# Kernel tuning notes

Measured on AMD Instinct MI355X. Metric: run time of the kernel, lower is better.

## Reference

```python
import jax, jax.numpy as jnp
import numpy as np

HIDDEN = 1024
HEADS = 16
HEAD = HIDDEN // HEADS
B, S = 2, 2048


def setup_inputs() -> dict:
    key = jax.random.key(0)
    ks = jax.random.split(key, 8)
    query = jax.random.normal(ks[0], (B, S, HIDDEN), dtype=jnp.float32)
    key_t = jax.random.normal(ks[1], (B, S, HIDDEN), dtype=jnp.float32)
    value = jax.random.normal(ks[2], (B, S, HIDDEN), dtype=jnp.float32)
    # causal mask, broadcastable over batch and heads; 0 -> masked (-inf)
    mask = jnp.tril(jnp.ones((S, S), dtype=jnp.int32))[None, None, :, :]
    # torch Linear weights are [out_features, in_features]
    scale = 0.02
    Wq = jax.random.normal(ks[3], (HIDDEN, HIDDEN), dtype=jnp.float32) * scale
    Wk = jax.random.normal(ks[4], (HIDDEN, HIDDEN), dtype=jnp.float32) * scale
    Wv = jax.random.normal(ks[5], (HIDDEN, HIDDEN), dtype=jnp.float32) * scale
    Wo = jax.random.normal(ks[6], (HIDDEN, HIDDEN), dtype=jnp.float32) * scale
    bo = jax.random.normal(ks[7], (HIDDEN,), dtype=jnp.float32) * scale
    return {"query": query, "key": key_t, "value": value, "mask": mask,
            "Wq": Wq, "Wk": Wk, "Wv": Wv, "Wo": Wo, "bo": bo}


def reference(query, key, value, mask, Wq, Wk, Wv, Wo, bo):
    b = query.shape[0]
    # Linear (no bias): x @ W^T, then split into heads -> [b, h, s, d]
    def heads(x, W):
        y = jnp.einsum('bse,oe->bso', x, W)
        return y.reshape(b, -1, HEADS, HEAD).transpose(0, 2, 1, 3)
    Q = heads(query, Wq)
    K = heads(key, Wk)
    V = heads(value, Wv)
    inv_scale = 1.0 / jnp.sqrt(jnp.float32(HEAD))
    scores = jnp.einsum('bhqd,bhkd->bhqk', Q, K) * inv_scale  # [b,h,s,s]
    scores = jnp.where(mask == 0, -jnp.inf, scores)
    attn = jax.nn.softmax(scores, axis=-1)
    x = jnp.einsum('bhqk,bhkd->bhqd', attn, V)
    x = x.transpose(0, 2, 1, 3).reshape(b, -1, HIDDEN)
    return jnp.einsum('bse,oe->bso', x, Wo) + bo
```

## Files before the change

### kernel.cpp

```cpp
#include <hip/hip_runtime.h>


typedef __attribute__((ext_vector_type(8))) short short8;
typedef __attribute__((ext_vector_type(4))) float f32x4;
typedef unsigned int u32;
typedef unsigned short u16;

__device__ inline f32x4 mfma16(short8 a, short8 b, f32x4 c) {
    return __builtin_amdgcn_mfma_f32_16x16x32_bf16(a, b, c, 0, 0, 0);
}
__device__ inline u16 f2bf(float f) {
    union { float f; u32 u; } v; v.f = f;
    u32 r = v.u + 0x7fff + ((v.u >> 16) & 1);
    return (u16)(r >> 16);
}
__device__ inline void gll16(void* lds, const void* g) {
    __builtin_amdgcn_global_load_lds((const __attribute__((address_space(1))) u32*)g,
                                     (__attribute__((address_space(3))) u32*)lds,
                                     16, 0, 0);
}
__device__ inline u32 pkbf(float hi, float lo) {
    return __builtin_amdgcn_perm(__float_as_uint(hi), __float_as_uint(lo),
                                 0x07060302u);
}

__global__ __launch_bounds__(256)
void cvt_all(const float* __restrict__ q, const float* __restrict__ k,
             const float* __restrict__ v, const float* __restrict__ wq,
             const float* __restrict__ wk, const float* __restrict__ wv,
             const float* __restrict__ wo,
             u16* __restrict__ q16, u16* __restrict__ k16,
             u16* __restrict__ v16, u16* __restrict__ w16) {
    const size_t QKV = 1u << 22;
    const size_t WSZ = 1u << 20;
    size_t base = ((size_t)blockIdx.x * 256 + threadIdx.x) * 8;
    const float* src; u16* dst; size_t off; float scale = 1.0f;
    if (base < QKV)            { src = q; dst = q16; off = base;
                                 scale = 0.125f * 1.44269504f; }
    else if (base < 2 * QKV)   { src = k; dst = k16; off = base - QKV;     }
    else if (base < 3 * QKV)   { src = v; dst = v16; off = base - 2 * QKV; }
    else {
        size_t wb = base - 3 * QKV;
        int wi = (int)(wb >> 20); off = wb & (WSZ - 1);
        src = wi == 0 ? wq : wi == 1 ? wk : wi == 2 ? wv : wo;
        dst = w16 + (size_t)wi * WSZ;
    }
    float4 f0 = *(const float4*)(src + off);
    float4 f1 = *(const float4*)(src + off + 4);
    short8 s = { (short)f2bf(f0.x * scale), (short)f2bf(f0.y * scale),
                 (short)f2bf(f0.z * scale), (short)f2bf(f0.w * scale),
                 (short)f2bf(f1.x * scale), (short)f2bf(f1.y * scale),
                 (short)f2bf(f1.z * scale), (short)f2bf(f1.w * scale) };
    *(short8*)(dst + off) = s;
}

__global__ __launch_bounds__(256)
void gemm_qkv(const u16* __restrict__ q16, const u16* __restrict__ k16,
              const u16* __restrict__ v16, const u16* __restrict__ w16,
              u16* __restrict__ Qg, u16* __restrict__ Kg, u16* __restrict__ Vt) {
    const int K = 1024;
    __shared__ u16 As[3][128 * 32];
    __shared__ u16 Bs[3][128 * 32];
    const int z = blockIdx.z;
    const u16* A = z == 0 ? q16 : z == 1 ? k16 : v16;
    const u16* W = w16 + (size_t)z * (1u << 20);

    const int tid = threadIdx.x, lane = tid & 63, w = tid >> 6;
    const int ln15 = lane & 15, quad = lane >> 4;
    const int fr = (ln15 >> 1) & 3;
    const int lrow = lane >> 2;
    const int lcs = (((lane & 3) ^ ((lane >> 3) & 3)) << 3);
    const int m0 = blockIdx.y * 128, n0 = blockIdx.x * 128;
    const int wm = (w >> 1) * 64, wn = (w & 1) * 64;

    f32x4 acc[4][4] = {};

    #pragma unroll
    for (int t = 0; t < 2; ++t)
        #pragma unroll
        for (int c = 0; c < 2; ++c) {
            gll16(&As[t][(w * 32 + c * 16) * 32],
                  &A[(size_t)(m0 + w * 32 + c * 16 + lrow) * K + t * 32 + lcs]);
            gll16(&Bs[t][(w * 32 + c * 16) * 32],
                  &W[(size_t)(n0 + w * 32 + c * 16 + lrow) * K + t * 32 + lcs]);
        }

    int cur = 0;
    for (int t = 0; t < 32; ++t) {
        if (t < 31) {
            __asm__ volatile("s_waitcnt vmcnt(4)" ::: "memory");
        } else {
            __asm__ volatile("s_waitcnt vmcnt(0)" ::: "memory");
        }
        __builtin_amdgcn_s_barrier();
        __builtin_amdgcn_sched_barrier(0);

        if (t < 30) {
            const int k0 = (t + 2) * 32;
            const int nb = (cur + 2 >= 3) ? cur - 1 : cur + 2;
            #pragma unroll
            for (int c = 0; c < 2; ++c) {
                gll16(&As[nb][(w * 32 + c * 16) * 32],
                      &A[(size_t)(m0 + w * 32 + c * 16 + lrow) * K + k0 + lcs]);
                gll16(&Bs[nb][(w * 32 + c * 16) * 32],
                      &W[(size_t)(n0 + w * 32 + c * 16 + lrow) * K + k0 + lcs]);
            }
        }
        __builtin_amdgcn_sched_barrier(0);

        short8 a[4], b[4];
        #pragma unroll
        for (int mt = 0; mt < 4; ++mt)
            a[mt] = *(const short8*)&As[cur][(wm + mt * 16 + ln15) * 32 +
                                            ((quad ^ fr) << 3)];
        #pragma unroll
        for (int nt = 0; nt < 4; ++nt)
            b[nt] = *(const short8*)&Bs[cur][(wn + nt * 16 + ln15) * 32 +
                                            ((quad ^ fr) << 3)];
        #pragma unroll
        for (int mt = 0; mt < 4; ++mt)
            #pragma unroll
            for (int nt = 0; nt < 4; ++nt)
                acc[mt][nt] = mfma16(a[mt], b[nt], acc[mt][nt]);

        cur = (cur == 2) ? 0 : cur + 1;
    }

    #pragma unroll
    for (int mt = 0; mt < 4; ++mt)
        #pragma unroll
        for (int nt = 0; nt < 4; ++nt)
            #pragma unroll
            for (int r = 0; r < 4; ++r) {
                int m = m0 + wm + mt * 16 + quad * 4 + r;
                int n = n0 + wn + nt * 16 + ln15;
                u16 hv = f2bf(acc[mt][nt][r]);
                if (z == 2) {
                    int b_ = m >> 11, s_ = m & 2047, h_ = n >> 6, d_ = n & 63;
                    int kl = s_ & 63;
                    int sp = (s_ & ~63) + (kl & 15) * 4 + (kl >> 4);
                    Vt[((size_t)(b_ * 16 + h_) * 64 + d_) * 2048 + sp] = hv;
                } else {
                    u16* dst = z ? Kg : Qg;
                    dst[(size_t)m * 1024 + n] = hv;
                }
            }
}

__global__ __launch_bounds__(256)
void gemm_out(const u16* __restrict__ A, const u16* __restrict__ W,
              const float* __restrict__ bias, float* __restrict__ out) {
    const int K = 1024;
    __shared__ u16 As[3][64 * 64];
    __shared__ u16 Bs[3][128 * 64];
    const int id = blockIdx.x;
    const int by = id >> 3, bx = id & 7;

    const int tid = threadIdx.x, lane = tid & 63, w = tid >> 6;
    const int ln15 = lane & 15, quad = lane >> 4, s7 = ln15 & 7;
    const int lr = lane >> 3;
    const int lcs = (((lane & 7) ^ lr) << 3);
    const int m0 = by * 64, n0 = bx * 128;
    const int wm = (w & 1) * 32, wn = (w >> 1) * 64;

    f32x4 acc[2][4] = {};

    #pragma unroll
    for (int t = 0; t < 2; ++t) {
        #pragma unroll
        for (int c = 0; c < 2; ++c)
            gll16(&As[t][(w * 16 + c * 8) * 64],
                  &A[(size_t)(m0 + w * 16 + c * 8 + lr) * K + t * 64 + lcs]);
        #pragma unroll
        for (int c = 0; c < 4; ++c)
            gll16(&Bs[t][(w * 32 + c * 8) * 64],
                  &W[(size_t)(n0 + w * 32 + c * 8 + lr) * K + t * 64 + lcs]);
    }

    int cur = 0;
    for (int i = 0; i < 16; ++i) {
        if (i < 15) {
            __asm__ volatile("s_waitcnt vmcnt(6)" ::: "memory");
        } else {
            __asm__ volatile("s_waitcnt vmcnt(0)" ::: "memory");
        }
        __builtin_amdgcn_s_barrier();
        __builtin_amdgcn_sched_barrier(0);

        if (i < 14) {
            const int k0 = (i + 2) * 64;
            const int nb = (cur + 2 >= 3) ? cur - 1 : cur + 2;
            #pragma unroll
            for (int c = 0; c < 2; ++c)
                gll16(&As[nb][(w * 16 + c * 8) * 64],
                      &A[(size_t)(m0 + w * 16 + c * 8 + lr) * K + k0 + lcs]);
            #pragma unroll
            for (int c = 0; c < 4; ++c)
                gll16(&Bs[nb][(w * 32 + c * 8) * 64],
                      &W[(size_t)(n0 + w * 32 + c * 8 + lr) * K + k0 + lcs]);
        }
        __builtin_amdgcn_sched_barrier(0);

        #pragma unroll
        for (int kh = 0; kh < 2; ++kh) {
            short8 a[2], b[4];
            #pragma unroll
            for (int mt = 0; mt < 2; ++mt)
                a[mt] = *(const short8*)&As[cur][(wm + mt * 16 + ln15) * 64 +
                                                (((kh * 4 + quad) ^ s7) << 3)];
            #pragma unroll
            for (int nt = 0; nt < 4; ++nt)
                b[nt] = *(const short8*)&Bs[cur][(wn + nt * 16 + ln15) * 64 +
                                                (((kh * 4 + quad) ^ s7) << 3)];
            #pragma unroll
            for (int mt = 0; mt < 2; ++mt)
                #pragma unroll
                for (int nt = 0; nt < 4; ++nt)
                    acc[mt][nt] = mfma16(a[mt], b[nt], acc[mt][nt]);
        }
        cur = (cur == 2) ? 0 : cur + 1;
    }

    #pragma unroll
    for (int mt = 0; mt < 2; ++mt)
        #pragma unroll
        for (int nt = 0; nt < 4; ++nt)
            #pragma unroll
            for (int r = 0; r < 4; ++r) {
                int m = m0 + wm + mt * 16 + quad * 4 + r;
                int n = n0 + wn + nt * 16 + ln15;
                out[(size_t)m * 1024 + n] = acc[mt][nt][r] + bias[n];
            }
}

__global__ __launch_bounds__(256)
void attn3(const u16* __restrict__ Qg, const u16* __restrict__ Kg,
           const u16* __restrict__ Vt, u16* __restrict__ Xb) {
    __shared__ u16 Kl[3][64 * 64];
    __shared__ u16 Vl[3][64 * 64];
    __shared__ u16 Pl[4][16 * 72];

    const int id = blockIdx.x;
    const int bh = id & 31, qt = 31 - (id >> 5);
    const int b = bh >> 4, h = bh & 15;
    const int tid = threadIdx.x, lane = tid & 63, w = tid >> 6;
    const int ln15 = lane & 15, quad = lane >> 4, s7 = ln15 & 7;
    const int lr = lane >> 3;
    const int lcs = (((lane & 7) ^ lr) << 3);
    const u16* Kbase = Kg + (size_t)b * 2048 * 1024 + h * 64;
    const u16* Vbase = Vt + (size_t)bh * 64 * 2048;
    const float M0L = 8.65617025f;
    const int q0 = qt * 64;

    const u16* qrow = Qg + (size_t)(b * 2048 + q0 + w * 16 + ln15) * 1024 + h * 64;
    short8 aq0 = *(const short8*)(qrow + quad * 8);
    short8 aq1 = *(const short8*)(qrow + 32 + quad * 8);
    __asm__ volatile("s_waitcnt vmcnt(0)" ::: "memory");

    f32x4 o[4] = {};
    float lsum[4] = {0.f, 0.f, 0.f, 0.f};

    #pragma unroll
    for (int c = 0; c < 2; ++c) {
        const int r0 = w * 16 + c * 8;
        gll16(&Kl[0][r0 * 64], Kbase + (size_t)(r0 + lr) * 1024 + lcs);
        gll16(&Vl[0][r0 * 64], Vbase + (size_t)(r0 + lr) * 2048 + lcs);
    }
    if (qt >= 1) {
        #pragma unroll
        for (int c = 0; c < 2; ++c) {
            const int r0 = w * 16 + c * 8;
            gll16(&Kl[1][r0 * 64], Kbase + (size_t)(64 + r0 + lr) * 1024 + lcs);
            gll16(&Vl[1][r0 * 64], Vbase + (size_t)(r0 + lr) * 2048 + 64 + lcs);
        }
    }

    int cur = 0;
    for (int kt = 0; kt <= qt; ++kt) {
        if (kt < qt) {
            __asm__ volatile("s_waitcnt vmcnt(4)" ::: "memory");
        } else {
            __asm__ volatile("s_waitcnt vmcnt(0)" ::: "memory");
        }
        __builtin_amdgcn_s_barrier();
        __builtin_amdgcn_sched_barrier(0);

        if (kt + 2 <= qt) {
            const int nk = (kt + 2) * 64;
            const int nb = (cur + 2 >= 3) ? cur - 1 : cur + 2;
            #pragma unroll
            for (int c = 0; c < 2; ++c) {
                const int r0 = w * 16 + c * 8;
                gll16(&Kl[nb][r0 * 64], Kbase + (size_t)(nk + r0 + lr) * 1024 + lcs);
                gll16(&Vl[nb][r0 * 64], Vbase + (size_t)(r0 + lr) * 2048 + nk + lcs);
            }
        }
        __builtin_amdgcn_sched_barrier(0);

        f32x4 sc[4];
        #pragma unroll
        for (int ct = 0; ct < 4; ++ct) {
            short8 b0 = *(const short8*)&Kl[cur][(ct * 16 + ln15) * 64 +
                                                ((quad ^ s7) << 3)];
            short8 b1 = *(const short8*)&Kl[cur][(ct * 16 + ln15) * 64 +
                                                (((4 + quad) ^ s7) << 3)];
            f32x4 c = {};
            c = mfma16(aq0, b0, c);
            c = mfma16(aq1, b1, c);
            sc[ct] = c;
        }

        const bool diag = (kt == qt);
        #pragma unroll
        for (int r = 0; r < 4; ++r) {
            float s0 = sc[0][r], s1 = sc[1][r], s2 = sc[2][r], s3 = sc[3][r];
            if (diag) {
                const int qq = w * 16 + quad * 4 + r;
                s0 = (ln15      <= qq) ? s0 : -1e30f;
                s1 = (16 + ln15 <= qq) ? s1 : -1e30f;
                s2 = (32 + ln15 <= qq) ? s2 : -1e30f;
                s3 = (48 + ln15 <= qq) ? s3 : -1e30f;
            }
            float p0 = __builtin_amdgcn_exp2f(s0 - M0L);
            float p1 = __builtin_amdgcn_exp2f(s1 - M0L);
            float p2 = __builtin_amdgcn_exp2f(s2 - M0L);
            float p3 = __builtin_amdgcn_exp2f(s3 - M0L);
            uint2 pw = make_uint2(pkbf(p1, p0), pkbf(p3, p2));
            *(uint2*)&Pl[w][(quad * 4 + r) * 72 + ln15 * 4] = pw;
            lsum[r] += (p0 + p1) + (p2 + p3);
        }

        __asm__ volatile("s_waitcnt lgkmcnt(0)" ::: "memory");
        short8 ap0 = *(const short8*)&Pl[w][ln15 * 72 + quad * 8];
        short8 ap1 = *(const short8*)&Pl[w][ln15 * 72 + 32 + quad * 8];

        #pragma unroll
        for (int dt = 0; dt < 4; ++dt) {
            short8 bv0 = *(const short8*)&Vl[cur][(dt * 16 + ln15) * 64 +
                                                 ((quad ^ s7) << 3)];
            short8 bv1 = *(const short8*)&Vl[cur][(dt * 16 + ln15) * 64 +
                                                 (((4 + quad) ^ s7) << 3)];
            o[dt] = mfma16(ap0, bv0, o[dt]);
            o[dt] = mfma16(ap1, bv1, o[dt]);
        }
        cur = (cur == 2) ? 0 : cur + 1;
    }

    #pragma unroll
    for (int r = 0; r < 4; ++r) {
        float l = lsum[r];
        #pragma unroll
        for (int off = 1; off < 16; off <<= 1)
            l += __shfl_xor(l, off);
        lsum[r] = l;
    }
    #pragma unroll
    for (int dt = 0; dt < 4; ++dt)
        #pragma unroll
        for (int r = 0; r < 4; ++r) {
            int q = q0 + w * 16 + quad * 4 + r;
            Xb[(size_t)(b * 2048 + q) * 1024 + h * 64 + dt * 16 + ln15] =
                f2bf(o[dt][r] / lsum[r]);
        }
}

extern "C" void kernel_launch(void* const* d_in, const int* in_sizes, int n_in,
                              void* d_out, int out_size, void* d_ws, size_t ws_size,
                              hipStream_t stream) {
    const float* query = (const float*)d_in[0];
    const float* key   = (const float*)d_in[1];
    const float* value = (const float*)d_in[2];
    const float* Wq = (const float*)d_in[4];
    const float* Wk = (const float*)d_in[5];
    const float* Wv = (const float*)d_in[6];
    const float* Wo = (const float*)d_in[7];
    const float* bo = (const float*)d_in[8];
    float* out = (float*)d_out;

    u16* ws  = (u16*)d_ws;
    const size_t T = 1ull << 22;
    u16* q16 = ws;
    u16* k16 = ws + T;
    u16* v16 = ws + 2 * T;
    u16* w16 = ws + 3 * T;
    u16* Qg  = ws + 4 * T;
    u16* Kg  = ws + 5 * T;
    u16* Vt  = (u16*)d_out;
    u16* Xb  = q16;
    const size_t WSZ = 1ull << 20;

    cvt_all<<<8192, 256, 0, stream>>>(query, key, value, Wq, Wk, Wv, Wo,
                                      q16, k16, v16, w16);

    gemm_qkv<<<dim3(8, 32, 3), 256, 0, stream>>>(q16, k16, v16, w16, Qg, Kg, Vt);

    attn3<<<1024, 256, 0, stream>>>(Qg, Kg, Vt, Xb);

    gemm_out<<<512, 256, 0, stream>>>(Xb, w16 + 3 * WSZ, bo, out);
}
```

Baseline: 223.3 us.

## Reshape QKV GEMM tile to 64x256 with double-buffered LDS

Changes the QKV projection block tile from 128x128 to 64x256, so each wave owns a 64x64 slice along N and all waves share the A tile. The LDS pipeline drops from triple to double buffering with a full vmcnt(0) wait every iteration, and the grid is reshaped to match. The aim is a different reuse and load balance with the same block count, but only one stage of prefetch is in flight, so global-load latency may be hidden less well.

Measured after the change: 225.9 us. Within noise of the previous version (+1.2%).

```diff
diff --git a/kernel.cpp b/kernel.cpp
--- a/kernel.cpp
+++ b/kernel.cpp
@@ -59,8 +59,8 @@
               const u16* __restrict__ v16, const u16* __restrict__ w16,
               u16* __restrict__ Qg, u16* __restrict__ Kg, u16* __restrict__ Vt) {
     const int K = 1024;
-    __shared__ u16 As[3][128 * 32];
-    __shared__ u16 Bs[3][128 * 32];
+    __shared__ u16 As[2][64 * 32];
+    __shared__ u16 Bs[2][256 * 32];
     const int z = blockIdx.z;
     const u16* A = z == 0 ? q16 : z == 1 ? k16 : v16;
     const u16* W = w16 + (size_t)z * (1u << 20);
@@ -70,48 +70,39 @@
     const int fr = (ln15 >> 1) & 3;
     const int lrow = lane >> 2;
     const int lcs = (((lane & 3) ^ ((lane >> 3) & 3)) << 3);
-    const int m0 = blockIdx.y * 128, n0 = blockIdx.x * 128;
-    const int wm = (w >> 1) * 64, wn = (w & 1) * 64;
+    const int m0 = blockIdx.y * 64, n0 = blockIdx.x * 256;
+    const int wn = w * 64;
 
     f32x4 acc[4][4] = {};
 
-    #pragma unroll
-    for (int t = 0; t < 2; ++t)
-        #pragma unroll
-        for (int c = 0; c < 2; ++c) {
-            gll16(&As[t][(w * 32 + c * 16) * 32],
-                  &A[(size_t)(m0 + w * 32 + c * 16 + lrow) * K + t * 32 + lcs]);
-            gll16(&Bs[t][(w * 32 + c * 16) * 32],
-                  &W[(size_t)(n0 + w * 32 + c * 16 + lrow) * K + t * 32 + lcs]);
-        }
-
-    int cur = 0;
+    gll16(&As[0][(w * 16) * 32],
+          &A[(size_t)(m0 + w * 16 + lrow) * K + lcs]);
+    #pragma unroll
+    for (int c = 0; c < 4; ++c)
+        gll16(&Bs[0][(wn + c * 16) * 32],
+              &W[(size_t)(n0 + wn + c * 16 + lrow) * K + lcs]);
+
     for (int t = 0; t < 32; ++t) {
+        const int cur = t & 1, nb = cur ^ 1;
+        __asm__ volatile("s_waitcnt vmcnt(0)" ::: "memory");
+        __builtin_amdgcn_s_barrier();
+        __builtin_amdgcn_sched_barrier(0);
+
         if (t < 31) {
-            __asm__ volatile("s_waitcnt vmcnt(4)" ::: "memory");
-        } else {
-            __asm__ volatile("s_waitcnt vmcnt(0)" ::: "memory");
-        }
-        __builtin_amdgcn_s_barrier();
-        __builtin_amdgcn_sched_barrier(0);
-
-        if (t < 30) {
-            const int k0 = (t + 2) * 32;
-            const int nb = (cur + 2 >= 3) ? cur - 1 : cur + 2;
-            #pragma unroll
-            for (int c = 0; c < 2; ++c) {
-                gll16(&As[nb][(w * 32 + c * 16) * 32],
-                      &A[(size_t)(m0 + w * 32 + c * 16 + lrow) * K + k0 + lcs]);
-                gll16(&Bs[nb][(w * 32 + c * 16) * 32],
-                      &W[(size_t)(n0 + w * 32 + c * 16 + lrow) * K + k0 + lcs]);
-            }
+            const int k0 = (t + 1) * 32;
+            gll16(&As[nb][(w * 16) * 32],
+                  &A[(size_t)(m0 + w * 16 + lrow) * K + k0 + lcs]);
+            #pragma unroll
+            for (int c = 0; c < 4; ++c)
+                gll16(&Bs[nb][(wn + c * 16) * 32],
+                      &W[(size_t)(n0 + wn + c * 16 + lrow) * K + k0 + lcs]);
         }
         __builtin_amdgcn_sched_barrier(0);
 
         short8 a[4], b[4];
         #pragma unroll
         for (int mt = 0; mt < 4; ++mt)
-            a[mt] = *(const short8*)&As[cur][(wm + mt * 16 + ln15) * 32 +
+            a[mt] = *(const short8*)&As[cur][(mt * 16 + ln15) * 32 +
                                             ((quad ^ fr) << 3)];
         #pragma unroll
         for (int nt = 0; nt < 4; ++nt)
@@ -122,8 +113,6 @@
             #pragma unroll
             for (int nt = 0; nt < 4; ++nt)
                 acc[mt][nt] = mfma16(a[mt], b[nt], acc[mt][nt]);
-
-        cur = (cur == 2) ? 0 : cur + 1;
     }
 
     #pragma unroll
@@ -132,7 +121,7 @@
         for (int nt = 0; nt < 4; ++nt)
             #pragma unroll
             for (int r = 0; r < 4; ++r) {
-                int m = m0 + wm + mt * 16 + quad * 4 + r;
+                int m = m0 + mt * 16 + quad * 4 + r;
                 int n = n0 + wn + nt * 16 + ln15;
                 u16 hv = f2bf(acc[mt][nt][r]);
                 if (z == 2) {
@@ -392,7 +381,7 @@
     cvt_all<<<8192, 256, 0, stream>>>(query, key, value, Wq, Wk, Wv, Wo,
                                       q16, k16, v16, w16);
 
-    gemm_qkv<<<dim3(8, 32, 3), 256, 0, stream>>>(q16, k16, v16, w16, Qg, Kg, Vt);
+    gemm_qkv<<<dim3(4, 64, 3), 256, 0, stream>>>(q16, k16, v16, w16, Qg, Kg, Vt);
 
     attn3<<<1024, 256, 0, stream>>>(Qg, Kg, Vt, Xb);
 
```
